# Performance work log

Measured on AMD Instinct MI355X. Metric: run time of the kernel, lower is better.

Reference implementation:

```python
import jax, jax.numpy as jnp
import numpy as np
from jax import lax

DN = ('NHWC', 'HWIO', 'NHWC')
EPS = 1e-3  # keras BatchNormalization default epsilon


def conv2d(x, w):
    return lax.conv_general_dilated(x, w, (1, 1), 'SAME', dimension_numbers=DN)


def convlstm2d(x, W, U, b):
    # x: (B,T,H,Wd,Cin); W: (kh,kw,Cin,4F); U: (kh,kw,F,4F); b: (4F,)
    # Keras ConvLSTM2D, gate order i,f,c,o; recurrent_activation=sigmoid, activation=relu
    B, T, H, Wd, _ = x.shape
    F = U.shape[2]
    xz = conv2d(x.reshape(B * T, H, Wd, -1), W).reshape(B, T, H, Wd, 4 * F) + b

    def step(carry, xt):
        h, c = carry
        z = xt + conv2d(h, U)
        i, f, g, o = jnp.split(z, 4, axis=-1)
        i = jax.nn.sigmoid(i)
        f = jax.nn.sigmoid(f)
        c = f * c + i * jax.nn.relu(g)
        h = jax.nn.sigmoid(o) * jax.nn.relu(c)
        return (h, c), h

    h0 = jnp.zeros((B, H, Wd, F), x.dtype)
    _, hs = lax.scan(step, (h0, h0), jnp.moveaxis(xz, 0, 1))  # (T,B,H,W,F)
    return jnp.moveaxis(hs, 0, 1)


def batchnorm(x, gamma, beta, mean, var):
    return (x - mean) * (gamma * lax.rsqrt(var + EPS)) + beta


def maxpool_122(x):
    # MaxPooling3D pool=(1,2,2), strides=(1,2,2), padding='same', channels_last
    return lax.reduce_window(x, -jnp.inf, lax.max, (1, 1, 2, 2, 1), (1, 1, 2, 2, 1), 'SAME')


def setup_inputs() -> dict:
    key = jax.random.key(0)
    ks = iter(jax.random.split(key, 32))
    s = 0.05
    d = {
        'x': jax.random.normal(next(ks), (8, 10, 64, 64, 3), jnp.float32),
        'W1': jax.random.normal(next(ks), (5, 5, 3, 128), jnp.float32) * s,
        'U1': jax.random.normal(next(ks), (5, 5, 32, 128), jnp.float32) * s,
        'b1': jnp.zeros((128,), jnp.float32),
        'g1': jax.random.uniform(next(ks), (32,), jnp.float32, 0.5, 1.5),
        'be1': jax.random.normal(next(ks), (32,), jnp.float32) * 0.1,
        'm1': jax.random.normal(next(ks), (32,), jnp.float32) * 0.1,
        'v1': jax.random.uniform(next(ks), (32,), jnp.float32, 0.5, 1.5),
        'W2': jax.random.normal(next(ks), (5, 5, 32, 128), jnp.float32) * s,
        'U2': jax.random.normal(next(ks), (5, 5, 32, 128), jnp.float32) * s,
        'b2': jnp.zeros((128,), jnp.float32),
        'g2': jax.random.uniform(next(ks), (32,), jnp.float32, 0.5, 1.5),
        'be2': jax.random.normal(next(ks), (32,), jnp.float32) * 0.1,
        'm2': jax.random.normal(next(ks), (32,), jnp.float32) * 0.1,
        'v2': jax.random.uniform(next(ks), (32,), jnp.float32, 0.5, 1.5),
        'W3': jax.random.normal(next(ks), (3, 3, 32, 128), jnp.float32) * s,
        'U3': jax.random.normal(next(ks), (3, 3, 32, 128), jnp.float32) * s,
        'b3': jnp.zeros((128,), jnp.float32),
        'g3': jax.random.uniform(next(ks), (32,), jnp.float32, 0.5, 1.5),
        'be3': jax.random.normal(next(ks), (32,), jnp.float32) * 0.1,
        'm3': jax.random.normal(next(ks), (32,), jnp.float32) * 0.1,
        'v3': jax.random.uniform(next(ks), (32,), jnp.float32, 0.5, 1.5),
        'Wd1': jax.random.normal(next(ks), (20480, 64), jnp.float32) * 0.01,
        'bd1': jnp.zeros((64,), jnp.float32),
        'Wd2': jax.random.normal(next(ks), (64, 10), jnp.float32) * 0.1,
        'bd2': jnp.zeros((10,), jnp.float32),
    }
    return d


def reference(x, W1, U1, b1, g1, be1, m1, v1, W2, U2, b2, g2, be2, m2, v2,
              W3, U3, b3, g3, be3, m3, v3, Wd1, bd1, Wd2, bd2):
    x = convlstm2d(x, W1, U1, b1)
    x = maxpool_122(batchnorm(x, g1, be1, m1, v1))
    x = convlstm2d(x, W2, U2, b2)
    x = maxpool_122(batchnorm(x, g2, be2, m2, v2))
    x = convlstm2d(x, W3, U3, b3)
    x = maxpool_122(batchnorm(x, g3, be3, m3, v3))
    x = x.reshape(x.shape[0], -1)  # (B, T*H*W*F) = (8, 20480)
    x = jax.nn.softmax(x @ Wd1 + bd1, axis=-1)
    return jax.nn.softmax(x @ Wd2 + bd2, axis=-1)
```

## Files before the change

kernel.cpp:

```cpp
#include <hip/hip_runtime.h>

using short8 = __attribute__((ext_vector_type(8))) short;
using f32x4  = __attribute__((ext_vector_type(4))) float;

__device__ __forceinline__ unsigned short f2bf(float x){
    unsigned u = __float_as_uint(x);
    unsigned r = (u + 0x7FFFu + ((u>>16)&1u)) >> 16;
    return (unsigned short)r;
}
__device__ __forceinline__ float bf2f(unsigned short h){
    return __uint_as_float(((unsigned)h)<<16);
}
__device__ __forceinline__ float sigf(float x){ return 1.0f/(1.0f+__expf(-x)); }
__device__ __forceinline__ int swz(int b){ return b ^ (((b>>7)&7)<<4); }

struct SP {
    const float *x;
    const float *g1,*be1,*m1,*v1;
    const float *g2,*be2,*m2,*v2;
    const float *g3,*be3,*m3,*v3;
    unsigned short *hs1,*hs2,*hs3;
    unsigned short *pl1,*pl2,*pl3;
    float *cst1,*cst2,*cst3;
    const short8 *U1b,*W1b,*U2b,*W2b,*U3b,*W3b;
    const float *bp;
};

__global__ __launch_bounds__(256)
void xform_all(const float* __restrict__ U1, const float* __restrict__ W1,
               const float* __restrict__ U2, const float* __restrict__ W2,
               const float* __restrict__ U3, const float* __restrict__ W3,
               const float* __restrict__ b1, const float* __restrict__ b2, const float* __restrict__ b3,
               short8* __restrict__ U1b, short8* __restrict__ W1b,
               short8* __restrict__ U2b, short8* __restrict__ W2b,
               short8* __restrict__ U3b, short8* __restrict__ W3b,
               float* __restrict__ bp)
{
    int i = blockIdx.x*256 + threadIdx.x;
    if (i >= 49536) return;
    if (i >= 49152) {
        int j = i - 49152, layer = j >> 7, np = j & 127;
        int oc = ((np>>4)&3)*32 + (np>>6)*16 + (np&15);
        const float* bs = layer==0 ? b1 : (layer==1 ? b2 : b3);
        bp[j] = bs[oc];
        return;
    }
    const float* src; short8* dst; int base, kmax;
    if      (i < 12800){ src=U1; dst=U1b; base=0;     kmax=800; }
    else if (i < 14336){ src=W1; dst=W1b; base=12800; kmax=75;  }
    else if (i < 27136){ src=U2; dst=U2b; base=14336; kmax=800; }
    else if (i < 39936){ src=W2; dst=W2b; base=27136; kmax=800; }
    else if (i < 44544){ src=U3; dst=U3b; base=39936; kmax=288; }
    else               { src=W3; dst=W3b; base=44544; kmax=288; }
    int j = i - base;
    int lane = j & 63, nt = (j >> 6) & 7, tap = j >> 9;
    int np = nt*16 + (lane & 15);
    int oc = ((np>>4)&3)*32 + (np>>6)*16 + (np&15);
    int g = lane >> 4;
    short8 pk;
    #pragma unroll
    for (int e = 0; e < 8; ++e) {
        int k = tap*32 + g*8 + e;
        unsigned short v = (k < kmax) ? f2bf(src[(long)k*128 + oc]) : (unsigned short)0;
        pk[e] = (short)v;
    }
    dst[j] = pk;
}

template<int MT2>
__device__ __forceinline__ void lstm_epilogue(
    f32x4 (&acc)[MT2][4], unsigned short* hs, float* cst, unsigned short* plout,
    const float* gg, const float* bb, const float* mm, const float* vv,
    int H, int W, int n, int y0, int x0, int t, int mh, int nh, int l15, int g4, int first)
{
    const int f = nh*16 + l15;
    const float sc = gg[f] * rsqrtf(vv[f] + 1e-3f);
    const float sh = bb[f] - mm[f]*sc;
    unsigned short* outh = hs + ((long)n*10 + t)*(long)H*W*32;
    float hv[MT2][4];
    #pragma unroll
    for (int mt = 0; mt < MT2; ++mt) {
        int row = y0 + mh*MT2 + mt;
        #pragma unroll
        for (int j = 0; j < 4; ++j) {
            int col = x0 + g4*4 + j;
            float zi = acc[mt][0][j];
            float zf = acc[mt][1][j];
            float zg = acc[mt][2][j];
            float zo = acc[mt][3][j];
            long cix = (((long)n*H + row)*W + col)*32 + f;
            float cold = first ? 0.0f : cst[cix];
            float cn = sigf(zf)*cold + sigf(zi)*fmaxf(zg, 0.0f);
            cst[cix] = cn;
            float h = sigf(zo)*fmaxf(cn, 0.0f);
            hv[mt][j] = h;
            outh[((long)row*W + col)*32 + f] = f2bf(h);
        }
    }
    #pragma unroll
    for (int mp = 0; mp < MT2/2; ++mp) {
        int orow = (y0>>1) + mh*(MT2/2) + mp;
        #pragma unroll
        for (int jp = 0; jp < 2; ++jp) {
            int ocol = (x0>>1) + g4*2 + jp;
            float mx = fmaxf(fmaxf(hv[2*mp][2*jp],   hv[2*mp][2*jp+1]),
                             fmaxf(hv[2*mp+1][2*jp], hv[2*mp+1][2*jp+1]));
            plout[(((long)(n*10 + t)*(H>>1) + orow)*(W>>1) + ocol)*32 + f] = f2bf(mx*sc + sh);
        }
    }
}

__device__ void l1_step(char* smem, const SP& p, int n, int y0, int x0, int t)
{
    constexpr int K = 5, TH = 8, PAD = 2, PH = 12, PW = 20, MT2 = 4, NTAP = 25, MPX = 128;
    const int H = 64, W = 64;
    unsigned short* patch_s = (unsigned short*)smem;
    unsigned short* xpk_s   = (unsigned short*)(smem + PH*PW*64);

    const int tid = threadIdx.x;
    const int lane = tid & 63, wid = tid >> 6;
    const int mh = wid >> 1, nh = wid & 1;
    const int l15 = lane & 15, g4 = lane >> 4;
    const int first = (t == 0);

    short8 z8 = {0,0,0,0,0,0,0,0};
    #pragma unroll 1
    for (int c = tid; c < MPX*96/8; c += 256)
        ((short8*)xpk_s)[c] = z8;

    if (!first) {
        const unsigned short* s = p.hs1 + ((long)n*10 + (t-1))*(long)H*W*32;
        #pragma unroll 1
        for (int c = tid; c < PH*PW*4; c += 256) {
            int pix = c >> 2, gq = c & 3;
            int pr = pix / PW, pc = pix % PW;
            int gy = y0 - PAD + pr, gx = x0 - PAD + pc;
            short8 v = z8;
            if ((unsigned)gy < (unsigned)H && (unsigned)gx < (unsigned)W)
                v = *(const short8*)(s + ((long)gy*W + gx)*32 + gq*8);
            *(short8*)((char*)patch_s + swz(pix*64 + gq*16)) = v;
        }
    }
    __syncthreads();
    {
        const float* xs = p.x + ((long)n*10 + t)*(long)H*W*3;
        #pragma unroll 1
        for (int c = tid; c < MPX*25; c += 256) {
            int px = c & (MPX-1), tap = c >> 7;
            int dy = tap/5, dx = tap - dy*5;
            int gy = y0 + (px>>4) - PAD + dy;
            int gx = x0 + (px&15) - PAD + dx;
            float v0=0.f, v1=0.f, v2=0.f;
            if ((unsigned)gy < (unsigned)H && (unsigned)gx < (unsigned)W) {
                const float* b = xs + ((long)gy*W + gx)*3;
                v0 = b[0]; v1 = b[1]; v2 = b[2];
            }
            int o = px*192 + tap*6;
            *(unsigned short*)((char*)xpk_s + swz(o))   = f2bf(v0);
            *(unsigned short*)((char*)xpk_s + swz(o+2)) = f2bf(v1);
            *(unsigned short*)((char*)xpk_s + swz(o+4)) = f2bf(v2);
        }
    }
    __syncthreads();

    f32x4 acc[MT2][4];
    #pragma unroll
    for (int ntl = 0; ntl < 4; ++ntl) {
        float bv = p.bp[(nh*4+ntl)*16 + l15];
        #pragma unroll
        for (int mt = 0; mt < MT2; ++mt)
            acc[mt][ntl] = (f32x4){bv,bv,bv,bv};
    }

    #pragma unroll 1
    for (int c = 0; c < 3; ++c) {
        const short8* wp = p.W1b + ((long)c*8 + nh*4)*64 + lane;
        short8 bf0 = wp[0], bf1 = wp[64], bf2 = wp[128], bf3 = wp[192];
        #pragma unroll
        for (int mt = 0; mt < MT2; ++mt) {
            short8 af = *(const short8*)((const char*)xpk_s +
                swz(((mh*MT2+mt)*16 + l15)*192 + c*64 + g4*16));
            acc[mt][0] = __builtin_amdgcn_mfma_f32_16x16x32_bf16(af, bf0, acc[mt][0], 0,0,0);
            acc[mt][1] = __builtin_amdgcn_mfma_f32_16x16x32_bf16(af, bf1, acc[mt][1], 0,0,0);
            acc[mt][2] = __builtin_amdgcn_mfma_f32_16x16x32_bf16(af, bf2, acc[mt][2], 0,0,0);
            acc[mt][3] = __builtin_amdgcn_mfma_f32_16x16x32_bf16(af, bf3, acc[mt][3], 0,0,0);
        }
    }
    if (!first) {
        const short8* ub = p.U1b + nh*4*64 + lane;
        short8 bA0 = ub[0], bA1 = ub[64], bA2 = ub[128], bA3 = ub[192];
        short8 bB0 = bA0, bB1 = bA1, bB2 = bA2, bB3 = bA3;
        { const short8* u = ub + 512; bB0=u[0]; bB1=u[64]; bB2=u[128]; bB3=u[192]; }
        #pragma unroll 1
        for (int tp = 0; tp < NTAP; tp += 2) {
            {
                int dy = tp / K, dx = tp % K;
                #pragma unroll
                for (int mt = 0; mt < MT2; ++mt) {
                    short8 af = *(const short8*)((const char*)patch_s +
                        swz(((mh*MT2 + mt + dy)*PW + l15 + dx)*64 + g4*16));
                    acc[mt][0] = __builtin_amdgcn_mfma_f32_16x16x32_bf16(af, bA0, acc[mt][0], 0,0,0);
                    acc[mt][1] = __builtin_amdgcn_mfma_f32_16x16x32_bf16(af, bA1, acc[mt][1], 0,0,0);
                    acc[mt][2] = __builtin_amdgcn_mfma_f32_16x16x32_bf16(af, bA2, acc[mt][2], 0,0,0);
                    acc[mt][3] = __builtin_amdgcn_mfma_f32_16x16x32_bf16(af, bA3, acc[mt][3], 0,0,0);
                }
                if (tp + 2 < NTAP) { const short8* u = ub + (long)(tp+2)*512; bA0=u[0];bA1=u[64];bA2=u[128];bA3=u[192]; }
            }
            if (tp + 1 < NTAP) {
                int dy = (tp+1) / K, dx = (tp+1) % K;
                #pragma unroll
                for (int mt = 0; mt < MT2; ++mt) {
                    short8 af = *(const short8*)((const char*)patch_s +
                        swz(((mh*MT2 + mt + dy)*PW + l15 + dx)*64 + g4*16));
                    acc[mt][0] = __builtin_amdgcn_mfma_f32_16x16x32_bf16(af, bB0, acc[mt][0], 0,0,0);
                    acc[mt][1] = __builtin_amdgcn_mfma_f32_16x16x32_bf16(af, bB1, acc[mt][1], 0,0,0);
                    acc[mt][2] = __builtin_amdgcn_mfma_f32_16x16x32_bf16(af, bB2, acc[mt][2], 0,0,0);
                    acc[mt][3] = __builtin_amdgcn_mfma_f32_16x16x32_bf16(af, bB3, acc[mt][3], 0,0,0);
                }
                if (tp + 3 < NTAP) { const short8* u = ub + (long)(tp+3)*512; bB0=u[0];bB1=u[64];bB2=u[128];bB3=u[192]; }
            }
        }
    }
    lstm_epilogue<MT2>(acc, p.hs1, p.cst1, p.pl1, p.g1, p.be1, p.m1, p.v1,
                       H, W, n, y0, x0, t, mh, nh, l15, g4, first);
}

template<int K, int HH>
__device__ void l23_step(char* smem, const SP& p,
    unsigned short* hs, const unsigned short* plin, unsigned short* plout, float* cst,
    const short8* Ufr, const short8* Wfr, const float* bp,
    const float* gg, const float* bb, const float* mm, const float* vv,
    int n, int y0, int x0, int t)
{
    constexpr int TH = 4, PAD = K/2, PH = TH+K-1, PW = 16+K-1, MT2 = 2, NTAP = K*K;
    const int H = HH, W = HH;
    unsigned short* patchH = (unsigned short*)smem;
    unsigned short* patchX = (unsigned short*)(smem + PH*PW*64);

    const int tid = threadIdx.x;
    const int lane = tid & 63, wid = tid >> 6;
    const int mh = wid >> 1, nh = wid & 1;
    const int l15 = lane & 15, g4 = lane >> 4;
    const int first = (t == 0);

    const unsigned short* hsrc = hs + ((long)n*10 + (t-1))*(long)H*W*32;
    const unsigned short* xsrc = plin + ((long)n*10 + t)*(long)H*W*32;
    short8 z8 = {0,0,0,0,0,0,0,0};
    #pragma unroll 1
    for (int c = tid; c < PH*PW*4; c += 256) {
        int pix = c >> 2, gq = c & 3;
        int pr = pix / PW, pc = pix % PW;
        int gy = y0 - PAD + pr, gx = x0 - PAD + pc;
        short8 vx = z8, vh = z8;
        if ((unsigned)gy < (unsigned)H && (unsigned)gx < (unsigned)W) {
            vx = *(const short8*)(xsrc + ((long)gy*W + gx)*32 + gq*8);
            if (!first) vh = *(const short8*)(hsrc + ((long)gy*W + gx)*32 + gq*8);
        }
        *(short8*)((char*)patchX + swz(pix*64 + gq*16)) = vx;
        *(short8*)((char*)patchH + swz(pix*64 + gq*16)) = vh;
    }
    __syncthreads();

    f32x4 acc[MT2][4];
    #pragma unroll
    for (int ntl = 0; ntl < 4; ++ntl) {
        float bv = bp[(nh*4+ntl)*16 + l15];
        #pragma unroll
        for (int mt = 0; mt < MT2; ++mt)
            acc[mt][ntl] = (f32x4){bv,bv,bv,bv};
    }

    auto tap_loop = [&](const unsigned short* patch, const short8* Wf) {
        const short8* ub = Wf + nh*4*64 + lane;
        short8 bA0 = ub[0], bA1 = ub[64], bA2 = ub[128], bA3 = ub[192];
        short8 bB0 = bA0, bB1 = bA1, bB2 = bA2, bB3 = bA3;
        { const short8* u = ub + 512; bB0=u[0]; bB1=u[64]; bB2=u[128]; bB3=u[192]; }
        #pragma unroll 1
        for (int tp = 0; tp < NTAP; tp += 2) {
            {
                int dy = tp / K, dx = tp % K;
                #pragma unroll
                for (int mt = 0; mt < MT2; ++mt) {
                    short8 af = *(const short8*)((const char*)patch +
                        swz(((mh*MT2 + mt + dy)*PW + l15 + dx)*64 + g4*16));
                    acc[mt][0] = __builtin_amdgcn_mfma_f32_16x16x32_bf16(af, bA0, acc[mt][0], 0,0,0);
                    acc[mt][1] = __builtin_amdgcn_mfma_f32_16x16x32_bf16(af, bA1, acc[mt][1], 0,0,0);
                    acc[mt][2] = __builtin_amdgcn_mfma_f32_16x16x32_bf16(af, bA2, acc[mt][2], 0,0,0);
                    acc[mt][3] = __builtin_amdgcn_mfma_f32_16x16x32_bf16(af, bA3, acc[mt][3], 0,0,0);
                }
                if (tp + 2 < NTAP) { const short8* u = ub + (long)(tp+2)*512; bA0=u[0];bA1=u[64];bA2=u[128];bA3=u[192]; }
            }
            if (tp + 1 < NTAP) {
                int dy = (tp+1) / K, dx = (tp+1) % K;
                #pragma unroll
                for (int mt = 0; mt < MT2; ++mt) {
                    short8 af = *(const short8*)((const char*)patch +
                        swz(((mh*MT2 + mt + dy)*PW + l15 + dx)*64 + g4*16));
                    acc[mt][0] = __builtin_amdgcn_mfma_f32_16x16x32_bf16(af, bB0, acc[mt][0], 0,0,0);
                    acc[mt][1] = __builtin_amdgcn_mfma_f32_16x16x32_bf16(af, bB1, acc[mt][1], 0,0,0);
                    acc[mt][2] = __builtin_amdgcn_mfma_f32_16x16x32_bf16(af, bB2, acc[mt][2], 0,0,0);
                    acc[mt][3] = __builtin_amdgcn_mfma_f32_16x16x32_bf16(af, bB3, acc[mt][3], 0,0,0);
                }
                if (tp + 3 < NTAP) { const short8* u = ub + (long)(tp+3)*512; bB0=u[0];bB1=u[64];bB2=u[128];bB3=u[192]; }
            }
        }
    };
    tap_loop(patchX, Wfr);
    if (!first) tap_loop(patchH, Ufr);

    lstm_epilogue<MT2>(acc, hs, cst, plout, gg, bb, mm, vv,
                       H, W, n, y0, x0, t, mh, nh, l15, g4, first);
}

__global__ __launch_bounds__(256)
void stage_k(SP p, int s)
{
    __shared__ __align__(16) char smem[40960];
    const int bid = blockIdx.x;
    if (bid < 256) {
        int t = s;
        if (t < 10) {
            int n = bid >> 5, rem = bid & 31;
            l1_step(smem, p, n, (rem >> 2)*8, (rem & 3)*16, t);
        }
    } else if (bid < 384) {
        int t = s - 1;
        if (t >= 0 && t < 10) {
            int idx = bid - 256;
            int n = idx >> 4, rem = idx & 15;
            l23_step<5,32>(smem, p, p.hs2, p.pl1, p.pl2, p.cst2,
                           p.U2b, p.W2b, p.bp + 128,
                           p.g2, p.be2, p.m2, p.v2,
                           n, (rem >> 1)*4, (rem & 1)*16, t);
        }
    } else {
        int t = s - 2;
        if (t >= 0 && t < 10) {
            int idx = bid - 384;
            int n = idx >> 2, rem = idx & 3;
            l23_step<3,16>(smem, p, p.hs3, p.pl2, p.pl3, p.cst3,
                           p.U3b, p.W3b, p.bp + 256,
                           p.g3, p.be3, p.m3, p.v3,
                           n, rem*4, 0, t);
        }
    }
}

__global__ __launch_bounds__(256)
void dense1(const unsigned short* __restrict__ flat, const float* __restrict__ Wd1,
            float* __restrict__ partial)
{
    __shared__ __align__(16) float xs[256*8];
    const int kc = blockIdx.x, k0 = kc*256;
    const int t = threadIdx.x;
    {
        int r = t >> 5, kb = (t & 31)*8;
        short8 v = *(const short8*)(flat + (long)r*20480 + k0 + kb);
        #pragma unroll
        for (int e = 0; e < 8; ++e) xs[(kb+e)*8 + r] = bf2f((unsigned short)v[e]);
    }
    __syncthreads();
    const int c = t & 63, seg = t >> 6;
    f32x4 accA = {0,0,0,0}, accB = {0,0,0,0};
    #pragma unroll 4
    for (int kk = seg*64; kk < seg*64 + 64; ++kk) {
        float w = Wd1[(long)(k0+kk)*64 + c];
        f32x4 xa = *(const f32x4*)&xs[kk*8];
        f32x4 xb = *(const f32x4*)&xs[kk*8 + 4];
        #pragma unroll
        for (int j = 0; j < 4; ++j) { accA[j] = fmaf(xa[j], w, accA[j]); accB[j] = fmaf(xb[j], w, accB[j]); }
    }
    __syncthreads();
    #pragma unroll
    for (int j = 0; j < 4; ++j) {
        xs[(seg*8 + j)*64 + c]     = accA[j];
        xs[(seg*8 + 4 + j)*64 + c] = accB[j];
    }
    __syncthreads();
    #pragma unroll
    for (int o = t; o < 512; o += 256) {
        int r = o >> 6, cc = o & 63;
        partial[(long)kc*512 + o] = (xs[(0*8+r)*64+cc] + xs[(1*8+r)*64+cc])
                                  + (xs[(2*8+r)*64+cc] + xs[(3*8+r)*64+cc]);
    }
}

__global__ __launch_bounds__(512)
void dense_tail(const float* __restrict__ partial, const float* __restrict__ bd1,
                const float* __restrict__ Wd2, const float* __restrict__ bd2,
                float* __restrict__ outp)
{
    __shared__ float d1[512];
    __shared__ float l2s[80];
    const int t = threadIdx.x;
    const int c = t & 63;
    float s = bd1[c];
    #pragma unroll 4
    for (int kc = 0; kc < 80; ++kc) s += partial[kc*512 + t];
    float mx = s;
    for (int o = 32; o > 0; o >>= 1) mx = fmaxf(mx, __shfl_xor(mx, o, 64));
    float e = __expf(s - mx);
    float sm = e;
    for (int o = 32; o > 0; o >>= 1) sm += __shfl_xor(sm, o, 64);
    d1[t] = e / sm;
    __syncthreads();
    if (t < 80) {
        int r = t / 10, o = t % 10;
        float l = bd2[o];
        #pragma unroll 8
        for (int cc = 0; cc < 64; ++cc) l = fmaf(d1[r*64 + cc], Wd2[cc*10 + o], l);
        l2s[t] = l;
    }
    __syncthreads();
    if (t < 8) {
        float mx2 = l2s[t*10];
        #pragma unroll
        for (int j = 1; j < 10; ++j) mx2 = fmaxf(mx2, l2s[t*10 + j]);
        float ev[10], s2 = 0.f;
        #pragma unroll
        for (int j = 0; j < 10; ++j) { ev[j] = __expf(l2s[t*10 + j] - mx2); s2 += ev[j]; }
        #pragma unroll
        for (int j = 0; j < 10; ++j) outp[t*10 + j] = ev[j] / s2;
    }
}

extern "C" void kernel_launch(void* const* d_in, const int* in_sizes, int n_in,
                              void* d_out, int out_size, void* d_ws, size_t ws_size,
                              hipStream_t stream)
{
    const float* x   = (const float*)d_in[0];
    const float* W1  = (const float*)d_in[1];
    const float* U1  = (const float*)d_in[2];
    const float* b1  = (const float*)d_in[3];
    const float* Wd1 = (const float*)d_in[22];
    const float* bd1 = (const float*)d_in[23];
    const float* Wd2 = (const float*)d_in[24];
    const float* bd2 = (const float*)d_in[25];

    char* ws = (char*)d_ws;
    SP p;
    p.x   = x;
    p.g1  = (const float*)d_in[4];  p.be1 = (const float*)d_in[5];  p.m1 = (const float*)d_in[6];  p.v1 = (const float*)d_in[7];
    p.g2  = (const float*)d_in[11]; p.be2 = (const float*)d_in[12]; p.m2 = (const float*)d_in[13]; p.v2 = (const float*)d_in[14];
    p.g3  = (const float*)d_in[18]; p.be3 = (const float*)d_in[19]; p.m3 = (const float*)d_in[20]; p.v3 = (const float*)d_in[21];

    p.hs1 = (unsigned short*)(ws);
    p.hs2 = (unsigned short*)(ws + 20971520);
    p.hs3 = (unsigned short*)(ws + 26214400);
    p.cst1 = (float*)(ws + 27525120);
    p.cst2 = (float*)(ws + 31719424);
    p.cst3 = (float*)(ws + 32768000);
    p.pl1 = (unsigned short*)(ws + 33030144);
    p.pl2 = (unsigned short*)(ws + 38273024);
    p.pl3 = (unsigned short*)(ws + 39583744);
    short8* U1b = (short8*)(ws + 39911424);
    short8* W1b = (short8*)(ws + 40116224);
    short8* U2b = (short8*)(ws + 40140800);
    short8* W2b = (short8*)(ws + 40345600);
    short8* U3b = (short8*)(ws + 40550400);
    short8* W3b = (short8*)(ws + 40624128);
    float*  bp  = (float*)(ws + 40697856);
    float*  partial = (float*)(ws + 40699392);
    p.U1b = U1b; p.W1b = W1b; p.U2b = U2b; p.W2b = W2b; p.U3b = U3b; p.W3b = W3b;
    p.bp = bp;

    xform_all<<<194, 256, 0, stream>>>(U1, W1,
        (const float*)d_in[9], (const float*)d_in[8],
        (const float*)d_in[16], (const float*)d_in[15],
        b1, (const float*)d_in[10], (const float*)d_in[17],
        U1b, W1b, U2b, W2b, U3b, W3b, bp);

    for (int s = 0; s < 12; ++s)
        stage_k<<<416, 256, 0, stream>>>(p, s);

    dense1<<<80, 256, 0, stream>>>(p.pl3, Wd1, partial);
    dense_tail<<<1, 512, 0, stream>>>(partial, bd1, Wd2, bd2, (float*)d_out);
}
```

Before: 237.8 us.

## Precompute layer-1 input conv in parallel kernel, shrink L1 tiles, fuse dense tail

The layer-1 input convolution (x*W1+b) now runs for all timesteps up front in a separate highly parallel kernel. Its result is stored as bf16 in a new workspace buffer, so each recurrent step only does the U1 recurrence. The layer-1 tiles shrink from 8 to 4 rows, doubling the block count and halving shared memory, and launch bounds request 2 blocks per CU. The two dense kernels are merged using an atomic last-block counter to drop one launch. This costs extra global traffic for the xz1 buffer plus bf16 rounding of the precomputed input projection.

Result: slower. 299.6 us (+26.0%).

```diff
diff --git a/kernel.cpp b/kernel.cpp
--- a/kernel.cpp
+++ b/kernel.cpp
@@ -1,6 +1,7 @@
 #include <hip/hip_runtime.h>
 
 using short8 = __attribute__((ext_vector_type(8))) short;
+using short4v = __attribute__((ext_vector_type(4))) short;
 using f32x4  = __attribute__((ext_vector_type(4))) float;
 
 __device__ __forceinline__ unsigned short f2bf(float x){
@@ -22,6 +23,7 @@
     unsigned short *hs1,*hs2,*hs3;
     unsigned short *pl1,*pl2,*pl3;
     float *cst1,*cst2,*cst3;
+    const unsigned short *xz1;
     const short8 *U1b,*W1b,*U2b,*W2b,*U3b,*W3b;
     const float *bp;
 };
@@ -67,6 +69,46 @@
     dst[j] = pk;
 }
 
+template<int K, int PW, int MT2>
+__device__ __forceinline__ void conv_taps(f32x4 (&acc)[MT2][4],
+    const unsigned short* patch, const short8* Wf, int mh, int nh, int l15, int g4, int lane)
+{
+    constexpr int NTAP = K*K;
+    const short8* ub = Wf + nh*4*64 + lane;
+    short8 bA0 = ub[0], bA1 = ub[64], bA2 = ub[128], bA3 = ub[192];
+    short8 bB0 = bA0, bB1 = bA1, bB2 = bA2, bB3 = bA3;
+    { const short8* u = ub + 512; bB0=u[0]; bB1=u[64]; bB2=u[128]; bB3=u[192]; }
+    #pragma unroll 1
+    for (int tp = 0; tp < NTAP; tp += 2) {
+        {
+            int dy = tp / K, dx = tp % K;
+            #pragma unroll
+            for (int mt = 0; mt < MT2; ++mt) {
+                short8 af = *(const short8*)((const char*)patch +
+                    swz(((mh*MT2 + mt + dy)*PW + l15 + dx)*64 + g4*16));
+                acc[mt][0] = __builtin_amdgcn_mfma_f32_16x16x32_bf16(af, bA0, acc[mt][0], 0,0,0);
+                acc[mt][1] = __builtin_amdgcn_mfma_f32_16x16x32_bf16(af, bA1, acc[mt][1], 0,0,0);
+                acc[mt][2] = __builtin_amdgcn_mfma_f32_16x16x32_bf16(af, bA2, acc[mt][2], 0,0,0);
+                acc[mt][3] = __builtin_amdgcn_mfma_f32_16x16x32_bf16(af, bA3, acc[mt][3], 0,0,0);
+            }
+            if (tp + 2 < NTAP) { const short8* u = ub + (long)(tp+2)*512; bA0=u[0];bA1=u[64];bA2=u[128];bA3=u[192]; }
+        }
+        if (tp + 1 < NTAP) {
+            int dy = (tp+1) / K, dx = (tp+1) % K;
+            #pragma unroll
+            for (int mt = 0; mt < MT2; ++mt) {
+                short8 af = *(const short8*)((const char*)patch +
+                    swz(((mh*MT2 + mt + dy)*PW + l15 + dx)*64 + g4*16));
+                acc[mt][0] = __builtin_amdgcn_mfma_f32_16x16x32_bf16(af, bB0, acc[mt][0], 0,0,0);
+                acc[mt][1] = __builtin_amdgcn_mfma_f32_16x16x32_bf16(af, bB1, acc[mt][1], 0,0,0);
+                acc[mt][2] = __builtin_amdgcn_mfma_f32_16x16x32_bf16(af, bB2, acc[mt][2], 0,0,0);
+                acc[mt][3] = __builtin_amdgcn_mfma_f32_16x16x32_bf16(af, bB3, acc[mt][3], 0,0,0);
+            }
+            if (tp + 3 < NTAP) { const short8* u = ub + (long)(tp+3)*512; bB0=u[0];bB1=u[64];bB2=u[128];bB3=u[192]; }
+        }
+    }
+}
+
 template<int MT2>
 __device__ __forceinline__ void lstm_epilogue(
     f32x4 (&acc)[MT2][4], unsigned short* hs, float* cst, unsigned short* plout,
@@ -110,40 +152,28 @@
     }
 }
 
-__device__ void l1_step(char* smem, const SP& p, int n, int y0, int x0, int t)
-{
-    constexpr int K = 5, TH = 8, PAD = 2, PH = 12, PW = 20, MT2 = 4, NTAP = 25, MPX = 128;
-    const int H = 64, W = 64;
-    unsigned short* patch_s = (unsigned short*)smem;
-    unsigned short* xpk_s   = (unsigned short*)(smem + PH*PW*64);
-
-    const int tid = threadIdx.x;
+__global__ __launch_bounds__(256)
+void xz1_pre(const float* __restrict__ x, const short8* __restrict__ W1b,
+             const float* __restrict__ bp, unsigned short* __restrict__ xz1)
+{
+    constexpr int PAD = 2, MPX = 128;
+    __shared__ __align__(16) unsigned short xpk_s[MPX*96];
+    const int bid = blockIdx.x, tid = threadIdx.x;
+    const int n = bid / 320, rem = bid % 320;
+    const int t = rem >> 5, tile = rem & 31;
+    const int y0 = (tile >> 2)*8, x0 = (tile & 3)*16;
+    const int xt = x0 >> 4;
     const int lane = tid & 63, wid = tid >> 6;
     const int mh = wid >> 1, nh = wid & 1;
     const int l15 = lane & 15, g4 = lane >> 4;
-    const int first = (t == 0);
 
     short8 z8 = {0,0,0,0,0,0,0,0};
     #pragma unroll 1
     for (int c = tid; c < MPX*96/8; c += 256)
         ((short8*)xpk_s)[c] = z8;
-
-    if (!first) {
-        const unsigned short* s = p.hs1 + ((long)n*10 + (t-1))*(long)H*W*32;
-        #pragma unroll 1
-        for (int c = tid; c < PH*PW*4; c += 256) {
-            int pix = c >> 2, gq = c & 3;
-            int pr = pix / PW, pc = pix % PW;
-            int gy = y0 - PAD + pr, gx = x0 - PAD + pc;
-            short8 v = z8;
-            if ((unsigned)gy < (unsigned)H && (unsigned)gx < (unsigned)W)
-                v = *(const short8*)(s + ((long)gy*W + gx)*32 + gq*8);
-            *(short8*)((char*)patch_s + swz(pix*64 + gq*16)) = v;
-        }
-    }
     __syncthreads();
     {
-        const float* xs = p.x + ((long)n*10 + t)*(long)H*W*3;
+        const float* xs = x + ((long)n*10 + t)*4096*3;
         #pragma unroll 1
         for (int c = tid; c < MPX*25; c += 256) {
             int px = c & (MPX-1), tap = c >> 7;
@@ -151,8 +181,8 @@
             int gy = y0 + (px>>4) - PAD + dy;
             int gx = x0 + (px&15) - PAD + dx;
             float v0=0.f, v1=0.f, v2=0.f;
-            if ((unsigned)gy < (unsigned)H && (unsigned)gx < (unsigned)W) {
-                const float* b = xs + ((long)gy*W + gx)*3;
+            if ((unsigned)gy < 64u && (unsigned)gx < 64u) {
+                const float* b = xs + ((long)gy*64 + gx)*3;
                 v0 = b[0]; v1 = b[1]; v2 = b[2];
             }
             int o = px*192 + tap*6;
@@ -163,64 +193,87 @@
     }
     __syncthreads();
 
-    f32x4 acc[MT2][4];
+    f32x4 acc[4][4];
     #pragma unroll
     for (int ntl = 0; ntl < 4; ++ntl) {
-        float bv = p.bp[(nh*4+ntl)*16 + l15];
-        #pragma unroll
-        for (int mt = 0; mt < MT2; ++mt)
+        float bv = bp[(nh*4+ntl)*16 + l15];
+        #pragma unroll
+        for (int mt = 0; mt < 4; ++mt)
             acc[mt][ntl] = (f32x4){bv,bv,bv,bv};
     }
-
     #pragma unroll 1
     for (int c = 0; c < 3; ++c) {
-        const short8* wp = p.W1b + ((long)c*8 + nh*4)*64 + lane;
+        const short8* wp = W1b + ((long)c*8 + nh*4)*64 + lane;
         short8 bf0 = wp[0], bf1 = wp[64], bf2 = wp[128], bf3 = wp[192];
         #pragma unroll
-        for (int mt = 0; mt < MT2; ++mt) {
+        for (int mt = 0; mt < 4; ++mt) {
             short8 af = *(const short8*)((const char*)xpk_s +
-                swz(((mh*MT2+mt)*16 + l15)*192 + c*64 + g4*16));
+                swz(((mh*4+mt)*16 + l15)*192 + c*64 + g4*16));
             acc[mt][0] = __builtin_amdgcn_mfma_f32_16x16x32_bf16(af, bf0, acc[mt][0], 0,0,0);
             acc[mt][1] = __builtin_amdgcn_mfma_f32_16x16x32_bf16(af, bf1, acc[mt][1], 0,0,0);
             acc[mt][2] = __builtin_amdgcn_mfma_f32_16x16x32_bf16(af, bf2, acc[mt][2], 0,0,0);
             acc[mt][3] = __builtin_amdgcn_mfma_f32_16x16x32_bf16(af, bf3, acc[mt][3], 0,0,0);
         }
     }
+    #pragma unroll
+    for (int mt = 0; mt < 4; ++mt) {
+        int row = y0 + mh*4 + mt;
+        long base = (((long)((n*10 + t)*64 + row))*4 + xt)*2048;
+        #pragma unroll
+        for (int ntl = 0; ntl < 4; ++ntl) {
+            int np = (nh*4+ntl)*16 + l15;
+            short4v s;
+            #pragma unroll
+            for (int j = 0; j < 4; ++j) s[j] = (short)f2bf(acc[mt][ntl][j]);
+            *(short4v*)&xz1[base + np*16 + g4*4] = s;
+        }
+    }
+}
+
+__device__ void l1_step(char* smem, const SP& p, int n, int y0, int x0, int t)
+{
+    constexpr int PAD = 2, PH = 8, PW = 20, MT2 = 2;
+    const int H = 64, W = 64;
+    unsigned short* patch_s = (unsigned short*)smem;
+    const int tid = threadIdx.x;
+    const int lane = tid & 63, wid = tid >> 6;
+    const int mh = wid >> 1, nh = wid & 1;
+    const int l15 = lane & 15, g4 = lane >> 4;
+    const int first = (t == 0);
+    const int xt = x0 >> 4;
+
     if (!first) {
-        const short8* ub = p.U1b + nh*4*64 + lane;
-        short8 bA0 = ub[0], bA1 = ub[64], bA2 = ub[128], bA3 = ub[192];
-        short8 bB0 = bA0, bB1 = bA1, bB2 = bA2, bB3 = bA3;
-        { const short8* u = ub + 512; bB0=u[0]; bB1=u[64]; bB2=u[128]; bB3=u[192]; }
+        const unsigned short* s = p.hs1 + ((long)n*10 + (t-1))*(long)H*W*32;
+        short8 z8 = {0,0,0,0,0,0,0,0};
         #pragma unroll 1
-        for (int tp = 0; tp < NTAP; tp += 2) {
-            {
-                int dy = tp / K, dx = tp % K;
-                #pragma unroll
-                for (int mt = 0; mt < MT2; ++mt) {
-                    short8 af = *(const short8*)((const char*)patch_s +
-                        swz(((mh*MT2 + mt + dy)*PW + l15 + dx)*64 + g4*16));
-                    acc[mt][0] = __builtin_amdgcn_mfma_f32_16x16x32_bf16(af, bA0, acc[mt][0], 0,0,0);
-                    acc[mt][1] = __builtin_amdgcn_mfma_f32_16x16x32_bf16(af, bA1, acc[mt][1], 0,0,0);
-                    acc[mt][2] = __builtin_amdgcn_mfma_f32_16x16x32_bf16(af, bA2, acc[mt][2], 0,0,0);
-                    acc[mt][3] = __builtin_amdgcn_mfma_f32_16x16x32_bf16(af, bA3, acc[mt][3], 0,0,0);
-                }
-                if (tp + 2 < NTAP) { const short8* u = ub + (long)(tp+2)*512; bA0=u[0];bA1=u[64];bA2=u[128];bA3=u[192]; }
-            }
-            if (tp + 1 < NTAP) {
-                int dy = (tp+1) / K, dx = (tp+1) % K;
-                #pragma unroll
-                for (int mt = 0; mt < MT2; ++mt) {
-                    short8 af = *(const short8*)((const char*)patch_s +
-                        swz(((mh*MT2 + mt + dy)*PW + l15 + dx)*64 + g4*16));
-                    acc[mt][0] = __builtin_amdgcn_mfma_f32_16x16x32_bf16(af, bB0, acc[mt][0], 0,0,0);
-                    acc[mt][1] = __builtin_amdgcn_mfma_f32_16x16x32_bf16(af, bB1, acc[mt][1], 0,0,0);
-                    acc[mt][2] = __builtin_amdgcn_mfma_f32_16x16x32_bf16(af, bB2, acc[mt][2], 0,0,0);
-                    acc[mt][3] = __builtin_amdgcn_mfma_f32_16x16x32_bf16(af, bB3, acc[mt][3], 0,0,0);
-                }
-                if (tp + 3 < NTAP) { const short8* u = ub + (long)(tp+3)*512; bB0=u[0];bB1=u[64];bB2=u[128];bB3=u[192]; }
-            }
-        }
-    }
+        for (int c = tid; c < PH*PW*4; c += 256) {
+            int pix = c >> 2, gq = c & 3;
+            int pr = pix / PW, pc = pix % PW;
+            int gy = y0 - PAD + pr, gx = x0 - PAD + pc;
+            short8 v = z8;
+            if ((unsigned)gy < 64u && (unsigned)gx < 64u)
+                v = *(const short8*)(s + ((long)gy*W + gx)*32 + gq*8);
+            *(short8*)((char*)patch_s + swz(pix*64 + gq*16)) = v;
+        }
+    }
+    __syncthreads();
+
+    f32x4 acc[MT2][4];
+    #pragma unroll
+    for (int mt = 0; mt < MT2; ++mt) {
+        int row = y0 + mh*MT2 + mt;
+        long base = (((long)((n*10 + t)*64 + row))*4 + xt)*2048;
+        #pragma unroll
+        for (int ntl = 0; ntl < 4; ++ntl) {
+            int np = (nh*4+ntl)*16 + l15;
+            short4v v = *(const short4v*)&p.xz1[base + np*16 + g4*4];
+            acc[mt][ntl] = (f32x4){bf2f((unsigned short)v[0]), bf2f((unsigned short)v[1]),
+                                   bf2f((unsigned short)v[2]), bf2f((unsigned short)v[3])};
+        }
+    }
+    if (!first)
+        conv_taps<5,PW,MT2>(acc, patch_s, p.U1b, mh, nh, l15, g4, lane);
+
     lstm_epilogue<MT2>(acc, p.hs1, p.cst1, p.pl1, p.g1, p.be1, p.m1, p.v1,
                        H, W, n, y0, x0, t, mh, nh, l15, g4, first);
 }
@@ -232,7 +285,7 @@
     const float* gg, const float* bb, const float* mm, const float* vv,
     int n, int y0, int x0, int t)
 {
-    constexpr int TH = 4, PAD = K/2, PH = TH+K-1, PW = 16+K-1, MT2 = 2, NTAP = K*K;
+    constexpr int TH = 4, PAD = K/2, PH = TH+K-1, PW = 16+K-1, MT2 = 2;
     const int H = HH, W = HH;
     unsigned short* patchH = (unsigned short*)smem;
     unsigned short* patchX = (unsigned short*)(smem + PH*PW*64);
@@ -269,64 +322,28 @@
         for (int mt = 0; mt < MT2; ++mt)
             acc[mt][ntl] = (f32x4){bv,bv,bv,bv};
     }
-
-    auto tap_loop = [&](const unsigned short* patch, const short8* Wf) {
-        const short8* ub = Wf + nh*4*64 + lane;
-        short8 bA0 = ub[0], bA1 = ub[64], bA2 = ub[128], bA3 = ub[192];
-        short8 bB0 = bA0, bB1 = bA1, bB2 = bA2, bB3 = bA3;
-        { const short8* u = ub + 512; bB0=u[0]; bB1=u[64]; bB2=u[128]; bB3=u[192]; }
-        #pragma unroll 1
-        for (int tp = 0; tp < NTAP; tp += 2) {
-            {
-                int dy = tp / K, dx = tp % K;
-                #pragma unroll
-                for (int mt = 0; mt < MT2; ++mt) {
-                    short8 af = *(const short8*)((const char*)patch +
-                        swz(((mh*MT2 + mt + dy)*PW + l15 + dx)*64 + g4*16));
-                    acc[mt][0] = __builtin_amdgcn_mfma_f32_16x16x32_bf16(af, bA0, acc[mt][0], 0,0,0);
-                    acc[mt][1] = __builtin_amdgcn_mfma_f32_16x16x32_bf16(af, bA1, acc[mt][1], 0,0,0);
-                    acc[mt][2] = __builtin_amdgcn_mfma_f32_16x16x32_bf16(af, bA2, acc[mt][2], 0,0,0);
-                    acc[mt][3] = __builtin_amdgcn_mfma_f32_16x16x32_bf16(af, bA3, acc[mt][3], 0,0,0);
-                }
-                if (tp + 2 < NTAP) { const short8* u = ub + (long)(tp+2)*512; bA0=u[0];bA1=u[64];bA2=u[128];bA3=u[192]; }
-            }
-            if (tp + 1 < NTAP) {
-                int dy = (tp+1) / K, dx = (tp+1) % K;
-                #pragma unroll
-                for (int mt = 0; mt < MT2; ++mt) {
-                    short8 af = *(const short8*)((const char*)patch +
-                        swz(((mh*MT2 + mt + dy)*PW + l15 + dx)*64 + g4*16));
-                    acc[mt][0] = __builtin_amdgcn_mfma_f32_16x16x32_bf16(af, bB0, acc[mt][0], 0,0,0);
-                    acc[mt][1] = __builtin_amdgcn_mfma_f32_16x16x32_bf16(af, bB1, acc[mt][1], 0,0,0);
-                    acc[mt][2] = __builtin_amdgcn_mfma_f32_16x16x32_bf16(af, bB2, acc[mt][2], 0,0,0);
-                    acc[mt][3] = __builtin_amdgcn_mfma_f32_16x16x32_bf16(af, bB3, acc[mt][3], 0,0,0);
-                }
-                if (tp + 3 < NTAP) { const short8* u = ub + (long)(tp+3)*512; bB0=u[0];bB1=u[64];bB2=u[128];bB3=u[192]; }
-            }
-        }
-    };
-    tap_loop(patchX, Wfr);
-    if (!first) tap_loop(patchH, Ufr);
+    conv_taps<K,PW,MT2>(acc, patchX, Wfr, mh, nh, l15, g4, lane);
+    if (!first) conv_taps<K,PW,MT2>(acc, patchH, Ufr, mh, nh, l15, g4, lane);
 
     lstm_epilogue<MT2>(acc, hs, cst, plout, gg, bb, mm, vv,
                        H, W, n, y0, x0, t, mh, nh, l15, g4, first);
 }
 
-__global__ __launch_bounds__(256)
+__global__ __launch_bounds__(256, 2)
 void stage_k(SP p, int s)
 {
-    __shared__ __align__(16) char smem[40960];
+    __shared__ __align__(16) char smem[20480];
     const int bid = blockIdx.x;
-    if (bid < 256) {
+    if (bid < 512) {
         int t = s;
         if (t < 10) {
-            int n = bid >> 5, rem = bid & 31;
-            l1_step(smem, p, n, (rem >> 2)*8, (rem & 3)*16, t);
-        }
-    } else if (bid < 384) {
+            int n = bid >> 6, rem = bid & 63;
+            l1_step(smem, p, n, (rem >> 2)*4, (rem & 3)*16, t);
+        }
+    } else if (bid < 640) {
         int t = s - 1;
         if (t >= 0 && t < 10) {
-            int idx = bid - 256;
+            int idx = bid - 512;
             int n = idx >> 4, rem = idx & 15;
             l23_step<5,32>(smem, p, p.hs2, p.pl1, p.pl2, p.cst2,
                            p.U2b, p.W2b, p.bp + 128,
@@ -336,7 +353,7 @@
     } else {
         int t = s - 2;
         if (t >= 0 && t < 10) {
-            int idx = bid - 384;
+            int idx = bid - 640;
             int n = idx >> 2, rem = idx & 3;
             l23_step<3,16>(smem, p, p.hs3, p.pl2, p.pl3, p.cst3,
                            p.U3b, p.W3b, p.bp + 256,
@@ -347,10 +364,13 @@
 }
 
 __global__ __launch_bounds__(256)
-void dense1(const unsigned short* __restrict__ flat, const float* __restrict__ Wd1,
-            float* __restrict__ partial)
-{
-    __shared__ __align__(16) float xs[256*8];
+void dense_all(const unsigned short* __restrict__ flat, const float* __restrict__ Wd1,
+               const float* __restrict__ bd1, const float* __restrict__ Wd2,
+               const float* __restrict__ bd2, float* __restrict__ partial,
+               unsigned* __restrict__ ctr, float* __restrict__ outp)
+{
+    __shared__ __align__(16) float xs[2048];
+    __shared__ unsigned rank_s;
     const int kc = blockIdx.x, k0 = kc*256;
     const int t = threadIdx.x;
     {
@@ -383,26 +403,31 @@
         partial[(long)kc*512 + o] = (xs[(0*8+r)*64+cc] + xs[(1*8+r)*64+cc])
                                   + (xs[(2*8+r)*64+cc] + xs[(3*8+r)*64+cc]);
     }
-}
-
-__global__ __launch_bounds__(512)
-void dense_tail(const float* __restrict__ partial, const float* __restrict__ bd1,
-                const float* __restrict__ Wd2, const float* __restrict__ bd2,
-                float* __restrict__ outp)
-{
-    __shared__ float d1[512];
-    __shared__ float l2s[80];
-    const int t = threadIdx.x;
-    const int c = t & 63;
-    float s = bd1[c];
-    #pragma unroll 4
-    for (int kc = 0; kc < 80; ++kc) s += partial[kc*512 + t];
-    float mx = s;
-    for (int o = 32; o > 0; o >>= 1) mx = fmaxf(mx, __shfl_xor(mx, o, 64));
-    float e = __expf(s - mx);
-    float sm = e;
-    for (int o = 32; o > 0; o >>= 1) sm += __shfl_xor(sm, o, 64);
-    d1[t] = e / sm;
+    __syncthreads();
+    if (t == 0) {
+        __builtin_amdgcn_fence(__ATOMIC_RELEASE, "agent");
+        rank_s = __hip_atomic_fetch_add(ctr, 1u, __ATOMIC_ACQ_REL, __HIP_MEMORY_SCOPE_AGENT);
+    }
+    __syncthreads();
+    if (rank_s != 79) return;
+    __builtin_amdgcn_fence(__ATOMIC_ACQUIRE, "agent");
+
+    float* d1  = xs;
+    float* l2s = xs + 512;
+    #pragma unroll
+    for (int rr = 0; rr < 2; ++rr) {
+        int idx = rr*256 + t;
+        int cc = idx & 63;
+        float s = bd1[cc];
+        #pragma unroll 4
+        for (int q = 0; q < 80; ++q) s += partial[q*512 + idx];
+        float mx = s;
+        for (int o = 32; o > 0; o >>= 1) mx = fmaxf(mx, __shfl_xor(mx, o, 64));
+        float e = __expf(s - mx);
+        float sm = e;
+        for (int o = 32; o > 0; o >>= 1) sm += __shfl_xor(sm, o, 64);
+        d1[idx] = e / sm;
+    }
     __syncthreads();
     if (t < 80) {
         int r = t / 10, o = t % 10;
@@ -429,9 +454,6 @@
                               hipStream_t stream)
 {
     const float* x   = (const float*)d_in[0];
-    const float* W1  = (const float*)d_in[1];
-    const float* U1  = (const float*)d_in[2];
-    const float* b1  = (const float*)d_in[3];
     const float* Wd1 = (const float*)d_in[22];
     const float* bd1 = (const float*)d_in[23];
     const float* Wd2 = (const float*)d_in[24];
@@ -453,26 +475,33 @@
     p.pl1 = (unsigned short*)(ws + 33030144);
     p.pl2 = (unsigned short*)(ws + 38273024);
     p.pl3 = (unsigned short*)(ws + 39583744);
-    short8* U1b = (short8*)(ws + 39911424);
-    short8* W1b = (short8*)(ws + 40116224);
-    short8* U2b = (short8*)(ws + 40140800);
-    short8* W2b = (short8*)(ws + 40345600);
-    short8* U3b = (short8*)(ws + 40550400);
-    short8* W3b = (short8*)(ws + 40624128);
-    float*  bp  = (float*)(ws + 40697856);
-    float*  partial = (float*)(ws + 40699392);
+    unsigned short* xz1 = (unsigned short*)(ws + 39911424);
+    short8* U1b = (short8*)(ws + 123797504);
+    short8* W1b = (short8*)(ws + 124002304);
+    short8* U2b = (short8*)(ws + 124026880);
+    short8* W2b = (short8*)(ws + 124231680);
+    short8* U3b = (short8*)(ws + 124436480);
+    short8* W3b = (short8*)(ws + 124510208);
+    float*  bp  = (float*)(ws + 124583936);
+    float*  partial = (float*)(ws + 124585472);
+    unsigned* ctr = (unsigned*)(ws + 124749312);
+    p.xz1 = xz1;
     p.U1b = U1b; p.W1b = W1b; p.U2b = U2b; p.W2b = W2b; p.U3b = U3b; p.W3b = W3b;
     p.bp = bp;
 
-    xform_all<<<194, 256, 0, stream>>>(U1, W1,
+    hipMemsetAsync(ctr, 0, 64, stream);
+
+    xform_all<<<194, 256, 0, stream>>>(
+        (const float*)d_in[2], (const float*)d_in[1],
         (const float*)d_in[9], (const float*)d_in[8],
         (const float*)d_in[16], (const float*)d_in[15],
-        b1, (const float*)d_in[10], (const float*)d_in[17],
+        (const float*)d_in[3], (const float*)d_in[10], (const float*)d_in[17],
         U1b, W1b, U2b, W2b, U3b, W3b, bp);
 
+    xz1_pre<<<2560, 256, 0, stream>>>(x, W1b, bp, xz1);
+
     for (int s = 0; s < 12; ++s)
-        stage_k<<<416, 256, 0, stream>>>(p, s);
-
-    dense1<<<80, 256, 0, stream>>>(p.pl3, Wd1, partial);
-    dense_tail<<<1, 512, 0, stream>>>(partial, bd1, Wd2, bd2, (float*)d_out);
-}
+        stage_k<<<672, 256, 0, stream>>>(p, s);
+
+    dense_all<<<80, 256, 0, stream>>>(p.pl3, Wd1, bd1, Wd2, bd2, partial, ctr, (float*)d_out);
+}
```
